# Kernel tuning notes

Measured on AMD Instinct MI355X. Metric: run time of the kernel, lower is better.

The kernel has to match this reference:

```python
import math
import jax, jax.numpy as jnp
import numpy as np

N, C, H, W = 32, 64, 96, 96
SHIFT_H, SHIFT_W = 1, -1  # fixed values of the random roll shifts

def _dwconv(x, w, dilation, pad):
    # depthwise conv, x: (n,c,h,w), w: (c,1,kh,kw)
    return jax.lax.conv_general_dilated(
        x, w, window_strides=(1, 1), padding=((pad, pad), (pad, pad)),
        rhs_dilation=(dilation, dilation),
        dimension_numbers=('NCHW', 'OIHW', 'NCHW'),
        feature_group_count=x.shape[1])

def _unfold_1x7_d2(x):
    # F.unfold(x, (1,7), dilation=(1,2), padding=(0,6)) -> (n,c,7,h,w)
    n, c, h, w = x.shape
    xp = jnp.pad(x, ((0, 0), (0, 0), (0, 0), (6, 6)))
    return jnp.stack([xp[..., 2 * k: 2 * k + w] for k in range(7)], axis=2)

def setup_inputs() -> dict:
    key = jax.random.key(0)
    k0, k1, k2, k3, k4, k5 = jax.random.split(key, 6)
    std = 0.1
    return {
        'x':  jax.random.normal(k0, (N, C, H, W), dtype=jnp.float32),
        'w3': jax.random.normal(k1, (C, 1, 5, 5), dtype=jnp.float32) * std,
        'w4': jax.random.normal(k2, (C, 1, 3, 3), dtype=jnp.float32) * std,
        'p5': jax.random.normal(k3, (1, C, C), dtype=jnp.float32) * std,
        'p6': jax.random.normal(k4, (C, 1), dtype=jnp.float32) * std,
        'p8': jax.random.normal(k5, (C, C * 7), dtype=jnp.float32) * std,
    }

def reference(x, w3, w4, p5, p6, p8):
    n, c, h, w = x.shape
    hw = h * w
    t0 = x
    t1 = jnp.roll(jnp.roll(t0, SHIFT_H, axis=2), SHIFT_W, axis=3)
    # channel attention: (n,c,c)
    t2 = jnp.einsum('nci,ndi->ncd', t0.reshape(n, c, hw), t1.reshape(n, c, hw)) / math.sqrt(hw)
    t3 = _dwconv(t1, w3, dilation=1, pad=2)          # (n,c,h,w)
    t4 = _dwconv(t1, w4, dilation=2, pad=2)          # (n,c,h,w)
    t5 = p5 * t2                                      # (n,c,c)
    t6 = jnp.einsum('nchw,ce->nehw', t4, p6).reshape(n, h, w)
    t7 = _unfold_1x7_d2(t0).reshape(n, c * 7, hw)     # (n, c*7, hw)
    t8 = jnp.einsum('nbc,bd->ndc', t5, p8)            # (n, c*7, c)
    t9 = jnp.einsum('nci,ni->nc', t3.reshape(n, c, hw), t6.reshape(n, hw)) / math.sqrt(hw)
    t10 = jnp.einsum('nkc,nks->ncs', t8, t7) / math.sqrt(c * 7)  # (n,c,hw)
    t11 = t9[:, :, None] + t10
    return t11.reshape(n, c, h, w)
```

## Files before the change

### kernel.cpp

```cpp
#include <hip/hip_runtime.h>

#define NB 32
#define CCH 64
#define HH 96
#define WWID 96
#define HWP (HH*WWID)
#define K7 448

#define OFF_T5 2097152
#define OFF_T8 2228224
#define OFF_T6 3145728
#define OFF_T9 3440640

typedef __attribute__((ext_vector_type(8))) short short8;
typedef __attribute__((ext_vector_type(4))) short shortx4;
typedef __attribute__((ext_vector_type(4))) float floatx4;
typedef float __attribute__((ext_vector_type(4), aligned(4))) float4u;

__device__ __forceinline__ short f2bf(float x) {
    unsigned u = __float_as_uint(x);
    unsigned r = (u + 0x7FFF + ((u >> 16) & 1)) >> 16;
    return (short)r;
}

__device__ __forceinline__ void ld_ab(const float* __restrict__ xa, int base,
                                      float4u* va, float4u* vb, int t) {
#pragma unroll
    for (int i = 0; i < 2; i++) {
        int idx = i * 256 + t;
        int c = idx >> 3, k4 = idx & 7;
        int gi = base + k4 * 4;
        const float* xc = xa + c * HWP;
        va[i] = *(const float4u*)(xc + gi);
        int h = gi / WWID, w = gi - h * WWID;
        int hr = (h == 0) ? (HH - 1) : (h - 1);
        const float* xrow = xc + hr * WWID;
        if (w < 92) {
            vb[i] = *(const float4u*)(xrow + w + 1);
        } else {
            float4u tmp;
            tmp.x = xrow[93]; tmp.y = xrow[94]; tmp.z = xrow[95]; tmp.w = xrow[0];
            vb[i] = tmp;
        }
    }
}

__global__ __launch_bounds__(256) void k_t2(const float* __restrict__ x,
                                            float* __restrict__ t2p) {
    int blk = blockIdx.x;
    int n = blk >> 4, sl = blk & 15;
    int k0 = sl * 576;
    __shared__ short ash[64][40];
    __shared__ short bsh[64][40];
    int t = threadIdx.x;
    int lane = t & 63, wv = t >> 6;
    int q = lane >> 4, r16 = lane & 15;
    const float* xa = x + (size_t)n * CCH * HWP;

    floatx4 acc[4] = {};

    float4u va[2], vb[2];
    ld_ab(xa, k0, va, vb, t);

    for (int kc = 0; kc < 576; kc += 32) {
        __syncthreads();
#pragma unroll
        for (int i = 0; i < 2; i++) {
            int idx = i * 256 + t;
            int c = idx >> 3, k4 = idx & 7;
            shortx4 pa = {f2bf(va[i].x), f2bf(va[i].y), f2bf(va[i].z), f2bf(va[i].w)};
            shortx4 pb = {f2bf(vb[i].x), f2bf(vb[i].y), f2bf(vb[i].z), f2bf(vb[i].w)};
            *(shortx4*)&ash[c][k4 * 4] = pa;
            *(shortx4*)&bsh[c][k4 * 4] = pb;
        }
        __syncthreads();
        if (kc + 32 < 576)
            ld_ab(xa, k0 + kc + 32, va, vb, t);
        short8 bfrag = *(const short8*)&bsh[wv * 16 + r16][q * 8];
#pragma unroll
        for (int mi = 0; mi < 4; mi++) {
            short8 afrag = *(const short8*)&ash[mi * 16 + r16][q * 8];
            acc[mi] = __builtin_amdgcn_mfma_f32_16x16x32_bf16(afrag, bfrag, acc[mi], 0, 0, 0);
        }
    }

    float* o = t2p + (size_t)(n * 16 + sl) * 4096;
#pragma unroll
    for (int mi = 0; mi < 4; mi++) {
        int m = mi * 16 + q * 4;
#pragma unroll
        for (int i = 0; i < 4; i++)
            o[(m + i) * 64 + wv * 16 + r16] = acc[mi][i];
    }
}

__global__ __launch_bounds__(256) void k_t5(const float* __restrict__ t2p,
                                            const float* __restrict__ p5,
                                            float* __restrict__ t5) {
    int idx = blockIdx.x * 256 + threadIdx.x;
    int n = idx >> 12, rc = idx & 4095;
    float s = 0.f;
#pragma unroll
    for (int sl = 0; sl < 16; sl++)
        s += t2p[((size_t)n * 16 + sl) * 4096 + rc];
    t5[idx] = s * p5[rc] * (1.0f / 96.0f);
}

__global__ __launch_bounds__(256) void k_t8(const float* __restrict__ t5,
                                            const float* __restrict__ p8,
                                            short* __restrict__ t8t) {
    int n = blockIdx.y;
    int idx = blockIdx.x * 256 + threadIdx.x;
    int k = idx >> 6, c = idx & 63;
    const float* t5n = t5 + (size_t)n * 4096;
    float s = 0.f;
#pragma unroll 8
    for (int b = 0; b < 64; b++)
        s += t5n[b * 64 + c] * p8[b * K7 + k];
    int c7 = k / 7, kk = k - c7 * 7;
    t8t[((size_t)n * 64 + c) * K7 + kk * 64 + c7] = f2bf(s * 0.04724555912f);
}

__global__ __launch_bounds__(256) void k_t6(const float* __restrict__ x,
                                            const float* __restrict__ w4,
                                            const float* __restrict__ p6,
                                            float* __restrict__ t6) {
    int n = blockIdx.y;
    int pix = blockIdx.x * 256 + threadIdx.x;
    int h = pix / WWID, w = pix - h * WWID;

    int off9[9];
    float m9[9];
#pragma unroll
    for (int i = 0; i < 3; i++) {
        int gh = h + (i - 1) * 2;
        bool vr = (gh >= 0) && (gh < HH);
        int srow = vr ? ((gh + HH - 1) % HH) * WWID : 0;
        float rm = vr ? 1.f : 0.f;
#pragma unroll
        for (int j = 0; j < 3; j++) {
            int gw = w + (j - 1) * 2;
            bool vc = (gw >= 0) && (gw < WWID);
            int scol = vc ? (gw + 1) % WWID : 0;
            off9[i * 3 + j] = srow + scol;
            m9[i * 3 + j] = vc ? rm : 0.f;
        }
    }
    const float* xn = x + (size_t)n * CCH * HWP;
    float acc = 0.f;
    for (int c = 0; c < CCH; c++) {
        const float* xc = xn + c * HWP;
        float pw = p6[c];
        const float* wc = w4 + c * 9;
#pragma unroll
        for (int ij = 0; ij < 9; ij++) {
            float wm = wc[ij] * pw * m9[ij];
            acc = fmaf(wm, xc[off9[ij]], acc);
        }
    }
    t6[(size_t)n * HWP + pix] = acc;
}

__global__ __launch_bounds__(256) void k_t9(const float* __restrict__ x,
                                            const float* __restrict__ w3,
                                            const float* __restrict__ t6,
                                            float* __restrict__ t9) {
    int n = blockIdx.y, c = blockIdx.x;
    __shared__ float xl[100][100];
    __shared__ float red[4];
    int t = threadIdx.x;
    const float* xc = x + ((size_t)n * CCH + c) * HWP;
    const float* t6n = t6 + (size_t)n * HWP;

    for (int idx = t; idx < 784; idx += 256) {
        if (idx < 400) {
            int r = idx / 100, col = idx - r * 100;
            int row = r < 2 ? r : r + 96;
            xl[row][col] = 0.f;
        } else {
            int rem = idx - 400;
            int h2 = rem >> 2, c4 = rem & 3;
            int col = c4 < 2 ? c4 : c4 + 96;
            xl[2 + h2][col] = 0.f;
        }
    }
    for (int idx = t; idx < HWP; idx += 256) {
        int h = idx / WWID, w = idx - h * WWID;
        int sh = (h == 0) ? (HH - 1) : (h - 1);
        int sw = (w == WWID - 1) ? 0 : (w + 1);
        xl[h + 2][w + 2] = xc[sh * WWID + sw];
    }
    float wv[25];
#pragma unroll
    for (int i = 0; i < 25; i++) wv[i] = w3[c * 25 + i];
    __syncthreads();

    float acc = 0.f;
#pragma unroll
    for (int g = 0; g < 9; g++) {
        int idx = g * 256 + t;
        int h = idx / 24, wg = idx - h * 24;
        int w0 = wg * 4;
        float4 tv = *(const float4*)(t6n + h * WWID + w0);
        float conv[4] = {0.f, 0.f, 0.f, 0.f};
#pragma unroll
        for (int kh = 0; kh < 5; kh++) {
            float4 ra = *(const float4*)&xl[h + kh][w0];
            float4 rb = *(const float4*)&xl[h + kh][w0 + 4];
            float r[8] = {ra.x, ra.y, ra.z, ra.w, rb.x, rb.y, rb.z, rb.w};
#pragma unroll
            for (int kw = 0; kw < 5; kw++) {
                float wk = wv[kh * 5 + kw];
                conv[0] = fmaf(wk, r[kw],     conv[0]);
                conv[1] = fmaf(wk, r[kw + 1], conv[1]);
                conv[2] = fmaf(wk, r[kw + 2], conv[2]);
                conv[3] = fmaf(wk, r[kw + 3], conv[3]);
            }
        }
        acc = fmaf(conv[0], tv.x, acc);
        acc = fmaf(conv[1], tv.y, acc);
        acc = fmaf(conv[2], tv.z, acc);
        acc = fmaf(conv[3], tv.w, acc);
    }
#pragma unroll
    for (int off = 32; off > 0; off >>= 1) acc += __shfl_down(acc, off, 64);
    if ((t & 63) == 0) red[t >> 6] = acc;
    __syncthreads();
    if (t == 0)
        t9[n * 64 + c] = (red[0] + red[1] + red[2] + red[3]) * (1.0f / 96.0f);
}

__global__ __launch_bounds__(256) void k_out(const float* __restrict__ x,
                                             const short* __restrict__ t8t,
                                             const float* __restrict__ t9,
                                             float* __restrict__ out) {
    int n = blockIdx.y;
    int h0 = blockIdx.x * 2;
    __shared__ short xsh[2 * 108 * 72];
    int t = threadIdx.x;

    for (int idx = t; idx < 2 * 12 * 72; idx += 256) {
        int r = idx / (12 * 72);
        int rem = idx - r * (12 * 72);
        int iwz = rem / 72, c7 = rem - iwz * 72;
        int iw = iwz < 6 ? iwz : iwz + 96;
        xsh[(r * 108 + iw) * 72 + c7] = 0;
    }
    const float* xn = x + (size_t)n * CCH * HWP;
    for (int idx = t; idx < 2 * CCH * WWID; idx += 256) {
        int r = idx / (CCH * WWID);
        int rem = idx - r * (CCH * WWID);
        int c7 = rem / WWID, w = rem - c7 * WWID;
        float v = xn[c7 * HWP + (h0 + r) * WWID + w];
        xsh[(r * 108 + w + 6) * 72 + c7] = f2bf(v);
    }
    __syncthreads();

    int lane = t & 63, wv = t >> 6;
    int q = lane >> 4, sl = lane & 15;
    floatx4 acc[4][3] = {};
    const short* A = t8t + (size_t)n * 64 * K7;

    for (int kc = 0; kc < K7; kc += 32) {
        int kk = kc >> 6;
        int c7b = (kc & 63) + q * 8;
        short8 a[4], b[3];
#pragma unroll
        for (int mi = 0; mi < 4; mi++)
            a[mi] = *(const short8*)(A + (mi * 16 + sl) * K7 + kc + q * 8);
#pragma unroll
        for (int sj = 0; sj < 3; sj++) {
            int si = wv * 3 + sj;
            int r = si >= 6 ? 1 : 0;
            int iw = (si - r * 6) * 16 + sl + 2 * kk;
            b[sj] = *(const short8*)&xsh[(r * 108 + iw) * 72 + c7b];
        }
#pragma unroll
        for (int mi = 0; mi < 4; mi++)
#pragma unroll
            for (int sj = 0; sj < 3; sj++)
                acc[mi][sj] = __builtin_amdgcn_mfma_f32_16x16x32_bf16(
                    a[mi], b[sj], acc[mi][sj], 0, 0, 0);
    }

    const float* t9n = t9 + n * 64;
#pragma unroll
    for (int mi = 0; mi < 4; mi++) {
#pragma unroll
        for (int i = 0; i < 4; i++) {
            int c = mi * 16 + q * 4 + i;
            float tv = t9n[c];
            float* orow = out + ((size_t)n * CCH + c) * HWP;
#pragma unroll
            for (int sj = 0; sj < 3; sj++) {
                int si = wv * 3 + sj;
                int r = si >= 6 ? 1 : 0;
                int w = (si - r * 6) * 16 + sl;
                orow[(h0 + r) * WWID + w] = acc[mi][sj][i] + tv;
            }
        }
    }
}

extern "C" void kernel_launch(void* const* d_in, const int* in_sizes, int n_in,
                              void* d_out, int out_size, void* d_ws, size_t ws_size,
                              hipStream_t stream) {
    const float* x  = (const float*)d_in[0];
    const float* w3 = (const float*)d_in[1];
    const float* w4 = (const float*)d_in[2];
    const float* p5 = (const float*)d_in[3];
    const float* p6 = (const float*)d_in[4];
    const float* p8 = (const float*)d_in[5];
    float* out = (float*)d_out;
    float* ws  = (float*)d_ws;

    float* t2p = ws;
    float* t5  = ws + OFF_T5;
    short* t8t = (short*)(ws + OFF_T8);
    float* t6  = ws + OFF_T6;
    float* t9  = ws + OFF_T9;

    k_t2<<<512, 256, 0, stream>>>(x, t2p);
    k_t5<<<512, 256, 0, stream>>>(t2p, p5, t5);
    k_t8<<<dim3(112, 32), 256, 0, stream>>>(t5, p8, t8t);
    k_t6<<<dim3(36, 32), 256, 0, stream>>>(x, w4, p6, t6);
    k_t9<<<dim3(64, 32), 256, 0, stream>>>(x, w3, t6, t9);
    k_out<<<dim3(48, 32), 256, 0, stream>>>(x, t8t, t9, out);
}
```

Measured before the change: 281.5 us.

## Double-buffer t2 global prefetch and XOR-swizzle the unfold LDS tile

In the channel-attention kernel, global loads now run two k-chunks ahead in a double register buffer instead of one, so load latency overlaps more MFMA work at the cost of more VGPRs. In the output kernel, the padded 72-short-stride LDS layout becomes a dense 64-short stride with an XOR swizzle on the channel index. The zero-padding columns move into a small shared region at the end. This shrinks LDS use and is meant to avoid bank conflicts on the 16-byte fragment reads, but it adds index arithmetic and a branch per B-fragment load.

```diff
diff --git a/kernel.cpp b/kernel.cpp
--- a/kernel.cpp
+++ b/kernel.cpp
@@ -59,23 +59,27 @@
 
     floatx4 acc[4] = {};
 
-    float4u va[2], vb[2];
-    ld_ab(xa, k0, va, vb, t);
+    float4u va[2][2], vb[2][2];
+    ld_ab(xa, k0,      va[0], vb[0], t);
+    ld_ab(xa, k0 + 32, va[1], vb[1], t);
 
     for (int kc = 0; kc < 576; kc += 32) {
+        int cur = (kc >> 5) & 1;
         __syncthreads();
 #pragma unroll
         for (int i = 0; i < 2; i++) {
             int idx = i * 256 + t;
             int c = idx >> 3, k4 = idx & 7;
-            shortx4 pa = {f2bf(va[i].x), f2bf(va[i].y), f2bf(va[i].z), f2bf(va[i].w)};
-            shortx4 pb = {f2bf(vb[i].x), f2bf(vb[i].y), f2bf(vb[i].z), f2bf(vb[i].w)};
+            shortx4 pa = {f2bf(va[cur][i].x), f2bf(va[cur][i].y),
+                          f2bf(va[cur][i].z), f2bf(va[cur][i].w)};
+            shortx4 pb = {f2bf(vb[cur][i].x), f2bf(vb[cur][i].y),
+                          f2bf(vb[cur][i].z), f2bf(vb[cur][i].w)};
             *(shortx4*)&ash[c][k4 * 4] = pa;
             *(shortx4*)&bsh[c][k4 * 4] = pb;
         }
         __syncthreads();
-        if (kc + 32 < 576)
-            ld_ab(xa, k0 + kc + 32, va, vb, t);
+        if (kc + 64 < 576)
+            ld_ab(xa, k0 + kc + 64, va[cur], vb[cur], t);
         short8 bfrag = *(const short8*)&bsh[wv * 16 + r16][q * 8];
 #pragma unroll
         for (int mi = 0; mi < 4; mi++) {
@@ -236,23 +240,19 @@
                                              float* __restrict__ out) {
     int n = blockIdx.y;
     int h0 = blockIdx.x * 2;
-    __shared__ short xsh[2 * 108 * 72];
+    __shared__ short xsh[204 * 64];
     int t = threadIdx.x;
 
-    for (int idx = t; idx < 2 * 12 * 72; idx += 256) {
-        int r = idx / (12 * 72);
-        int rem = idx - r * (12 * 72);
-        int iwz = rem / 72, c7 = rem - iwz * 72;
-        int iw = iwz < 6 ? iwz : iwz + 96;
-        xsh[(r * 108 + iw) * 72 + c7] = 0;
-    }
+    for (int idx = t; idx < 12 * 64; idx += 256) xsh[192 * 64 + idx] = 0;
+
     const float* xn = x + (size_t)n * CCH * HWP;
     for (int idx = t; idx < 2 * CCH * WWID; idx += 256) {
         int r = idx / (CCH * WWID);
         int rem = idx - r * (CCH * WWID);
         int c7 = rem / WWID, w = rem - c7 * WWID;
         float v = xn[c7 * HWP + (h0 + r) * WWID + w];
-        xsh[(r * 108 + w + 6) * 72 + c7] = f2bf(v);
+        int R = r * 96 + w;
+        xsh[R * 64 + (c7 ^ ((R & 7) << 3))] = f2bf(v);
     }
     __syncthreads();
 
@@ -273,7 +273,9 @@
             int si = wv * 3 + sj;
             int r = si >= 6 ? 1 : 0;
             int iw = (si - r * 6) * 16 + sl + 2 * kk;
-            b[sj] = *(const short8*)&xsh[(r * 108 + iw) * 72 + c7b];
+            int Rv = (iw >= 6 && iw < 102) ? (r * 96 + iw - 6)
+                                           : (192 + (iw < 6 ? iw : iw - 96));
+            b[sj] = *(const short8*)&xsh[Rv * 64 + (c7b ^ ((Rv & 7) << 3))];
         }
 #pragma unroll
         for (int mi = 0; mi < 4; mi++)
```

Measured after the change: 296.3 us. 1.05x slower.

## Vectorize x staging loads and retile k_out MFMA warp work as 2x6

Applied to the files above, without the earlier changes.

The shared-memory staging of x in k_out now reads float4 vectors from global memory instead of scalar floats, which cuts the number of load instructions. The MFMA tiling per wave changes from 4 channel tiles by 3 spatial tiles to 2 channel tiles by 6 spatial tiles. Each wave now owns one output row and half of the channels, which changes how many A loads come from global memory versus B loads from LDS. The scattered bf16 stores into LDS with a stride of 72 may still cause bank conflicts.

```diff
diff --git a/kernel.cpp b/kernel.cpp
--- a/kernel.cpp
+++ b/kernel.cpp
@@ -247,57 +247,58 @@
         xsh[(r * 108 + iw) * 72 + c7] = 0;
     }
     const float* xn = x + (size_t)n * CCH * HWP;
-    for (int idx = t; idx < 2 * CCH * WWID; idx += 256) {
-        int r = idx / (CCH * WWID);
-        int rem = idx - r * (CCH * WWID);
-        int c7 = rem / WWID, w = rem - c7 * WWID;
-        float v = xn[c7 * HWP + (h0 + r) * WWID + w];
-        xsh[(r * 108 + w + 6) * 72 + c7] = f2bf(v);
+    for (int idx = t; idx < 2 * CCH * 24; idx += 256) {
+        int r = idx / (CCH * 24);
+        int rem = idx - r * (CCH * 24);
+        int c7 = rem / 24, wb = rem - c7 * 24;
+        int w0 = wb * 4;
+        float4 v = *(const float4*)(xn + c7 * HWP + (h0 + r) * WWID + w0);
+        int base = (r * 108 + w0 + 6) * 72 + c7;
+        xsh[base]       = f2bf(v.x);
+        xsh[base + 72]  = f2bf(v.y);
+        xsh[base + 144] = f2bf(v.z);
+        xsh[base + 216] = f2bf(v.w);
     }
     __syncthreads();
 
     int lane = t & 63, wv = t >> 6;
     int q = lane >> 4, sl = lane & 15;
-    floatx4 acc[4][3] = {};
+    int mh = wv & 1;
+    int sh2 = wv >> 1;
+    floatx4 acc[2][6] = {};
     const short* A = t8t + (size_t)n * 64 * K7;
 
     for (int kc = 0; kc < K7; kc += 32) {
         int kk = kc >> 6;
         int c7b = (kc & 63) + q * 8;
-        short8 a[4], b[3];
-#pragma unroll
-        for (int mi = 0; mi < 4; mi++)
-            a[mi] = *(const short8*)(A + (mi * 16 + sl) * K7 + kc + q * 8);
-#pragma unroll
-        for (int sj = 0; sj < 3; sj++) {
-            int si = wv * 3 + sj;
-            int r = si >= 6 ? 1 : 0;
-            int iw = (si - r * 6) * 16 + sl + 2 * kk;
-            b[sj] = *(const short8*)&xsh[(r * 108 + iw) * 72 + c7b];
-        }
-#pragma unroll
-        for (int mi = 0; mi < 4; mi++)
-#pragma unroll
-            for (int sj = 0; sj < 3; sj++)
+        short8 a[2], b[6];
+#pragma unroll
+        for (int mi = 0; mi < 2; mi++)
+            a[mi] = *(const short8*)(A + ((mh * 2 + mi) * 16 + sl) * K7 + kc + q * 8);
+#pragma unroll
+        for (int sj = 0; sj < 6; sj++) {
+            int iw = sj * 16 + sl + 2 * kk;
+            b[sj] = *(const short8*)&xsh[(sh2 * 108 + iw) * 72 + c7b];
+        }
+#pragma unroll
+        for (int mi = 0; mi < 2; mi++)
+#pragma unroll
+            for (int sj = 0; sj < 6; sj++)
                 acc[mi][sj] = __builtin_amdgcn_mfma_f32_16x16x32_bf16(
                     a[mi], b[sj], acc[mi][sj], 0, 0, 0);
     }
 
     const float* t9n = t9 + n * 64;
 #pragma unroll
-    for (int mi = 0; mi < 4; mi++) {
+    for (int mi = 0; mi < 2; mi++) {
 #pragma unroll
         for (int i = 0; i < 4; i++) {
-            int c = mi * 16 + q * 4 + i;
+            int c = (mh * 2 + mi) * 16 + q * 4 + i;
             float tv = t9n[c];
-            float* orow = out + ((size_t)n * CCH + c) * HWP;
-#pragma unroll
-            for (int sj = 0; sj < 3; sj++) {
-                int si = wv * 3 + sj;
-                int r = si >= 6 ? 1 : 0;
-                int w = (si - r * 6) * 16 + sl;
-                orow[(h0 + r) * WWID + w] = acc[mi][sj][i] + tv;
-            }
+            float* orow = out + ((size_t)n * CCH + c) * HWP + (h0 + sh2) * WWID;
+#pragma unroll
+            for (int sj = 0; sj < 6; sj++)
+                orow[sj * 16 + sl] = acc[mi][sj][i] + tv;
         }
     }
 }
```

After: 270.8 us. -3.8%, faster.
